# Kernel tuning notes

Measured on AMD Instinct MI355X. Metric: run time of the kernel, lower is better.

The kernel has to match this reference:

```python
import jax, jax.numpy as jnp
import numpy as np

B, N, T, D = 8, 32, 64, 64            # batch, nodes, time steps, node_dims
K, H, SO, HF = 4, 256, 256, 256       # edge_types, sep_hidden, sep_out, fusion hidden
E = N * (N - 1)                        # fully connected, no self loops


def setup_inputs() -> dict:
    key = jax.random.key(0)
    ks = jax.random.split(key, 12)
    inputs = jax.random.normal(ks[0], (B, N, T, D), jnp.float32)
    rel_type = jax.nn.softmax(jax.random.normal(ks[1], (B, E, K), jnp.float32), axis=-1)
    off = np.array([(i, j) for i in range(N) for j in range(N) if i != j])
    eye = np.eye(N, dtype=np.float32)
    send_mask = jnp.asarray(eye[off[:, 0]])  # [E, N] one-hot senders
    rec_mask = jnp.asarray(eye[off[:, 1]])   # [E, N] one-hot receivers
    s = 0.05
    W1 = jax.random.normal(ks[2], (K, 2 * D, H), jnp.float32) * s
    b1 = jnp.zeros((K, H), jnp.float32)
    W2 = jax.random.normal(ks[3], (K, H, SO), jnp.float32) * s
    b2 = jnp.zeros((K, SO), jnp.float32)
    Wf1 = jax.random.normal(ks[4], (D + SO, HF), jnp.float32) * s
    bf1 = jnp.zeros((HF,), jnp.float32)
    Wf2 = jax.random.normal(ks[5], (HF, HF), jnp.float32) * s
    bf2 = jnp.zeros((HF,), jnp.float32)
    Wf3 = jax.random.normal(ks[6], (HF, D), jnp.float32) * s
    bf3 = jnp.zeros((D,), jnp.float32)
    return dict(inputs=inputs, rel_type=rel_type, send_mask=send_mask, rec_mask=rec_mask,
                W1=W1, b1=b1, W2=W2, b2=b2, Wf1=Wf1, bf1=bf1, Wf2=Wf2, bf2=bf2,
                Wf3=Wf3, bf3=bf3, pred_steps=1)


def reference(inputs, rel_type, send_mask, rec_mask, W1, b1, W2, b2,
              Wf1, bf1, Wf2, bf2, Wf3, bf3, pred_steps):
    # inputs: [B, N, T, D] -> [B, T, N, D]
    x = jnp.swapaxes(inputs, 1, 2)
    t_full = x.shape[1]

    def one_step(node_input, rel):
        # NOTE: the original forward swaps send/rec masks when calling
        # one_step_ahead; reproduced faithfully here.
        send_b = jnp.einsum('en,btnd->bted', rec_mask, node_input)
        rec_b = jnp.einsum('en,btnd->bted', send_mask, node_input)
        edge_rep = jnp.concatenate([send_b, rec_b], axis=-1)  # [B,Tm,E,2D]
        fused = jnp.zeros(edge_rep.shape[:-1] + (SO,), edge_rep.dtype)
        for i in range(K):  # skip_first=False -> start at 0
            h = jax.nn.relu(edge_rep @ W1[i] + b1[i])
            h = jax.nn.relu(h @ W2[i] + b2[i])
            fused = fused + h * rel[..., i:i + 1]
        # aggregate edges -> nodes (original uses the swapped 'rec_mask',
        # which is forward's send_mask)
        agg = jnp.einsum('bted,en->btnd', fused, send_mask)
        aug = jnp.concatenate([node_input, agg], axis=-1)  # [B,Tm,N,D+SO]
        p = jax.nn.relu(aug @ Wf1 + bf1)
        p = jax.nn.relu(p @ Wf2 + bf2)
        p = p @ Wf3 + bf3
        return node_input + p

    last_pred = x[:, 0::pred_steps]                    # [B, Tm, N, D]
    curr_rel = jnp.broadcast_to(rel_type[:, None], (x.shape[0], t_full, E, K))[:, 0::pred_steps]
    preds = []
    for _ in range(pred_steps):
        last_pred = one_step(last_pred, curr_rel)
        preds.append(last_pred)
    # interleave preds back onto the original time grid
    stacked = jnp.stack(preds, axis=2)                 # [B, Tm, pred_steps, N, D]
    out = stacked.reshape(stacked.shape[0], -1, N, D)  # [B, Tm*pred_steps, N, D]
    pred_all = out[:, :t_full - 1]
    return jnp.swapaxes(pred_all, 1, 2)                # [B, N, T-1, D]
```

## Files before the change

### kernel.cpp

```cpp
#include <hip/hip_runtime.h>
#include <hip/hip_fp16.h>

typedef _Float16 f16;
typedef _Float16 f16x8 __attribute__((ext_vector_type(8)));
typedef _Float16 f16x4 __attribute__((ext_vector_type(4)));
typedef float    f32x4 __attribute__((ext_vector_type(4)));

#define AS1 __attribute__((address_space(1)))
#define AS3 __attribute__((address_space(3)))

__device__ __forceinline__ void gl_lds16(const void* g, void* l) {
    __builtin_amdgcn_global_load_lds((const AS1 unsigned int*)g,
                                     (AS3 unsigned int*)l, 16, 0, 0);
}

#define NB   8
#define NN   32
#define NT   64
#define ND   64
#define NK   4
#define NH   256
#define NSO  256
#define NE   992
#define TOUT 63
#define M1   (NB*TOUT*NN)
#define NBT  (NB*TOUT)

static constexpr size_t SZ_RS   = (size_t)M1 * 1024 * 2;
static constexpr size_t OFF_R   = 0;
static constexpr size_t OFF_S   = OFF_R + SZ_RS;
static constexpr size_t OFF_W2T = OFF_S + SZ_RS;
static constexpr size_t OFF_WF1 = OFF_W2T + 4*256*256*2;
static constexpr size_t OFF_WF2 = OFF_WF1 + 256*320*2;
static constexpr size_t OFF_WF3 = OFF_WF2 + 256*256*2;
static constexpr size_t OFF_REL = OFF_WF3 + 64*256*2;
static constexpr size_t OFF_AGG = OFF_REL + (size_t)NB*NN*NK*32*4;
static constexpr size_t OFF_W1T = OFF_AGG + (size_t)M1*256*4;

__global__ __launch_bounds__(256) void k0_prep(
    const float* __restrict__ W1, const float* __restrict__ W2,
    const float* __restrict__ Wf1, const float* __restrict__ Wf2,
    const float* __restrict__ Wf3, const float* __restrict__ rel,
    f16* __restrict__ W1T, f16* __restrict__ W2T, f16* __restrict__ Wf1T,
    f16* __restrict__ Wf2T, f16* __restrict__ Wf3T, float* __restrict__ REL,
    unsigned int* __restrict__ AGGZ)
{
    int id = blockIdx.x * 256 + threadIdx.x;
    if (id < 262144) {
        int k = id >> 16, co = (id >> 8) & 255, h = id & 255;
        W2T[id] = (f16)W2[k*65536 + h*256 + co];
    } else if (id < 344064) {
        int i = id - 262144; int co = i / 320, d = i % 320;
        Wf1T[i] = (f16)Wf1[d*256 + co];
    } else if (id < 409600) {
        int i = id - 344064; int co = i >> 8, h = i & 255;
        Wf2T[i] = (f16)Wf2[h*256 + co];
    } else if (id < 425984) {
        int i = id - 409600; int d = i >> 8, h = i & 255;
        Wf3T[i] = (f16)Wf3[h*64 + d];
    } else if (id < 458752) {
        int i = id - 425984;
        int j = i & 31, k = (i >> 5) & 3, ns = (i >> 7) & 31, b = i >> 12;
        float v = 0.f;
        if (j != ns) v = rel[(b*NE + ns*31 + (j < ns ? j : j - 1))*NK + k];
        REL[i] = v;
    } else {
        int i = id - 458752;
        int c = i >> 6, d = i & 63;
        int k = c >> 9, dd = (c >> 8) & 1, h = c & 255;
        W1T[i] = (f16)W1[(k*128 + dd*64 + d)*NH + h];
    }
    #pragma unroll
    for (int j = 0; j < 7; ++j) {
        int idx = id + j*589824;
        if (idx < 4128768) AGGZ[idx] = 0u;
    }
}

__global__ __launch_bounds__(256) void k1_partials(
    const float* __restrict__ inputs, const f16* __restrict__ W1T,
    const float* __restrict__ b1, f16* __restrict__ Rb, f16* __restrict__ Sb)
{
    __shared__ __align__(16) f16 xs[64][72];
    __shared__ __align__(16) f16 wl[256][72];
    int tid = threadIdx.x;
    int w = tid >> 6, lane = tid & 63, ln = lane & 15, q = lane >> 4;
    int m0 = blockIdx.x * 64;

    #pragma unroll
    for (int it = 0; it < 2; ++it) {
        int idx8 = it*256 + tid;
        int m = idx8 >> 3, hs = idx8 & 7;
        int mrow = m0 + m;
        int b = mrow / 2016, r2 = mrow % 2016, t = r2 >> 5, n = r2 & 31;
        const float* px = &inputs[((b*NN + n)*NT + t)*ND + hs*8];
        f32x4 v0 = *(const f32x4*)px, v1 = *(const f32x4*)(px + 4);
        f16x8 o;
        #pragma unroll
        for (int e = 0; e < 4; ++e) { o[e] = (f16)v0[e]; o[e+4] = (f16)v1[e]; }
        *(f16x8*)&xs[m][hs*8] = o;
    }
    const f32x4 z4 = {0.f, 0.f, 0.f, 0.f};
    for (int cc = 0; cc < 8; ++cc) {
        int k = cc >> 1, dd = cc & 1;
        __syncthreads();
        #pragma unroll
        for (int it = 0; it < 8; ++it) {
            int idx8 = it*256 + tid;
            int co = idx8 >> 3, seg = idx8 & 7;
            *(f16x8*)&wl[co][seg*8] = *(const f16x8*)&W1T[(size_t)(cc*256 + co)*64 + seg*8];
        }
        __syncthreads();
        f32x4 acc[16];
        #pragma unroll
        for (int nt = 0; nt < 16; ++nt) acc[nt] = z4;
        #pragma unroll
        for (int ks = 0; ks < 2; ++ks) {
            f16x8 Af = *(const f16x8*)&xs[w*16 + ln][ks*32 + q*8];
            #pragma unroll
            for (int nt = 0; nt < 16; ++nt) {
                f16x8 Bf = *(const f16x8*)&wl[nt*16 + ln][ks*32 + q*8];
                acc[nt] = __builtin_amdgcn_mfma_f32_16x16x32_f16(Af, Bf, acc[nt], 0, 0, 0);
            }
        }
        __syncthreads();
        f16* ob = &wl[0][0];
        #pragma unroll
        for (int nt = 0; nt < 16; ++nt) {
            int co = nt*16 + ln;
            float bias = dd ? b1[k*NH + co] : 0.f;
            #pragma unroll
            for (int r = 0; r < 4; ++r) {
                float v = acc[nt][r] + bias;
                ob[(w*16 + q*4 + r)*264 + co] = (f16)v;
            }
        }
        __syncthreads();
        f16* dst = dd ? Sb : Rb;
        #pragma unroll
        for (int it = 0; it < 8; ++it) {
            int idx8 = it*256 + tid;
            int m = idx8 >> 5, seg = idx8 & 31;
            int hcb = seg >> 3, c = seg & 7;
            *(f16x8*)&dst[(size_t)(m0 + m)*1024 + k*256 + hcb*64 + c*8] =
                *(const f16x8*)&ob[m*264 + hcb*64 + (((c ^ (m & 7))) << 3)];
        }
    }
}

__global__ __launch_bounds__(512, 2) void k2_edge(
    const f16* __restrict__ Rb, const f16* __restrict__ Sb,
    const f16* __restrict__ W2T, const float* __restrict__ b2,
    const float* __restrict__ REL, float* __restrict__ AGG)
{
    __shared__ __align__(16) f16 Rbuf[2][32*256];
    __shared__ __align__(16) f16 Sbuf[2][4*256];
    int tid = threadIdx.x;
    int blk = blockIdx.x;
    int k = blk & 3, g = blk >> 2;
    int w = tid >> 6, lane = tid & 63, ln = lane & 15, q = lane >> 4;
    int mg = w >> 2, ng = w & 3;
    int lrow = lane >> 5, lseg = lane & 31;

    f16x8 Breg[4][8];
    float bias[4];
    #pragma unroll
    for (int nt = 0; nt < 4; ++nt) {
        int co = ng*64 + nt*16 + ln;
        bias[nt] = b2[k*256 + co];
        const f16* wrow = &W2T[(size_t)(k*256 + co)*256];
        #pragma unroll
        for (int ks = 0; ks < 8; ++ks)
            Breg[nt][ks] = *(const f16x8*)&wrow[ks*32 + q*8];
    }

    auto stageR = [&](int bt, int buf) {
        #pragma unroll
        for (int it = 0; it < 2; ++it) {
            int rowbase = (w*2 + it)*2;
            gl_lds16(&Rb[((size_t)bt*NN + rowbase + lrow)*1024 + k*256 + lseg*8],
                     &Rbuf[buf][rowbase*256 + lane*8]);
        }
    };
    auto stageS = [&](int i, int buf) {
        int bt = g*8 + (i >> 3), nsq = i & 7;
        if (w < 2)
            gl_lds16(&Sb[((size_t)bt*NN + nsq*4 + w*2 + lrow)*1024 + k*256 + lseg*8],
                     &Sbuf[buf][(w*2)*256 + lane*8]);
    };

    stageR(g*8, 0);
    stageS(0, 0);
    __syncthreads();

    const f32x4 z4 = {0.f, 0.f, 0.f, 0.f};
    for (int i = 0; i < 64; ++i) {
        int ibt = i >> 3, nsq = i & 7;
        int bt = g*8 + ibt, b = bt / TOUT;
        int rb = ibt & 1, sb = i & 1;
        if (i < 63) stageS(i + 1, sb ^ 1);
        if (nsq == 6 && ibt < 7) stageR(bt + 1, rb ^ 1);

        const f16* Rl = &Rbuf[rb][0];
        const f16* Sl = &Sbuf[sb][0];
        int ns0 = nsq*4 + mg*2;
        f32x4 acc[4][4];
        #pragma unroll
        for (int mt = 0; mt < 4; ++mt)
            #pragma unroll
            for (int nt = 0; nt < 4; ++nt) acc[mt][nt] = z4;

        #pragma unroll
        for (int ks = 0; ks < 8; ++ks) {
            int hc = ks >> 1;
            int c4 = (ks & 1)*4 + q;
            int paR = hc*64 + ((c4 ^ (ln & 7)) << 3);
            f16x8 rlo = *(const f16x8*)&Rl[ln*256 + paR];
            f16x8 rhi = *(const f16x8*)&Rl[(16 + ln)*256 + paR];
            f16x8 s0 = *(const f16x8*)&Sl[(mg*2 + 0)*256 + hc*64 + ((c4 ^ (ns0 & 7)) << 3)];
            f16x8 s1 = *(const f16x8*)&Sl[(mg*2 + 1)*256 + hc*64 + ((c4 ^ ((ns0 + 1) & 7)) << 3)];
            f16x8 A[4];
            #pragma unroll
            for (int mt = 0; mt < 4; ++mt) {
                f16x8 rr = (mt & 1) ? rhi : rlo;
                f16x8 ss = (mt >> 1) ? s1 : s0;
                f16x8 v;
                #pragma unroll
                for (int e = 0; e < 8; ++e) {
                    f16 x = rr[e] + ss[e];
                    v[e] = x > (f16)0 ? x : (f16)0;
                }
                A[mt] = v;
            }
            #pragma unroll
            for (int nt = 0; nt < 4; ++nt) {
                f16x8 Bf = Breg[nt][ks];
                #pragma unroll
                for (int mt = 0; mt < 4; ++mt)
                    acc[mt][nt] = __builtin_amdgcn_mfma_f32_16x16x32_f16(
                        A[mt], Bf, acc[mt][nt], 0, 0, 0);
            }
        }
        #pragma unroll
        for (int half = 0; half < 2; ++half) {
            int ns = ns0 + half;
            const float* relp = &REL[(((size_t)b*NN + ns)*NK + k)*32];
            f32x4 rel0 = *(const f32x4*)&relp[q*4];
            f32x4 rel1 = *(const f32x4*)&relp[16 + q*4];
            #pragma unroll
            for (int nt = 0; nt < 4; ++nt) {
                float s = 0.f;
                #pragma unroll
                for (int r = 0; r < 4; ++r) {
                    float v0 = acc[2*half + 0][nt][r] + bias[nt];
                    float v1 = acc[2*half + 1][nt][r] + bias[nt];
                    v0 = v0 > 0.f ? v0 : 0.f;
                    v1 = v1 > 0.f ? v1 : 0.f;
                    s += v0 * rel0[r] + v1 * rel1[r];
                }
                s += __shfl_xor(s, 16);
                s += __shfl_xor(s, 32);
                if (lane < 16)
                    atomicAdd(&AGG[((size_t)bt*NN + ns)*256 + ng*64 + nt*16 + lane], s);
            }
        }
        __syncthreads();
    }
}

__global__ __launch_bounds__(256) void k3_node(
    const float* __restrict__ inputs, const float* __restrict__ AGG,
    const f16* __restrict__ Wf1T, const float* __restrict__ bf1,
    const f16* __restrict__ Wf2T, const float* __restrict__ bf2,
    const f16* __restrict__ Wf3T, const float* __restrict__ bf3,
    float* __restrict__ out)
{
    __shared__ __align__(16) f16 aug[64][328];
    __shared__ __align__(16) f16 p1[64][264];
    __shared__ __align__(16) f16 wl[256][72];
    int tid = threadIdx.x;
    int w = tid >> 6, lane = tid & 63, ln = lane & 15, q = lane >> 4;
    int m0 = blockIdx.x * 64;

    for (int it = 0; it < 10; ++it) {
        int s = it*256 + tid;
        if (s < 512) {
            int m = s >> 3, hs = s & 7;
            int mrow = m0 + m;
            int b = mrow / 2016, r2 = mrow % 2016, t = r2 >> 5, n = r2 & 31;
            const float* px = &inputs[((b*NN + n)*NT + t)*ND + hs*8];
            f32x4 v0 = *(const f32x4*)px, v1 = *(const f32x4*)(px + 4);
            f16x8 o;
            #pragma unroll
            for (int e = 0; e < 4; ++e) { o[e] = (f16)v0[e]; o[e+4] = (f16)v1[e]; }
            *(f16x8*)&aug[m][hs*8] = o;
        } else {
            int s2 = s - 512;
            int m = s2 >> 5, hs = s2 & 31;
            const float* pa = &AGG[(size_t)(m0 + m)*NSO + hs*8];
            f32x4 v0 = *(const f32x4*)pa, v1 = *(const f32x4*)(pa + 4);
            f16x8 o;
            #pragma unroll
            for (int e = 0; e < 4; ++e) { o[e] = (f16)v0[e]; o[e+4] = (f16)v1[e]; }
            *(f16x8*)&aug[m][64 + hs*8] = o;
        }
    }
    const f32x4 z4 = {0.f, 0.f, 0.f, 0.f};
    f32x4 acc1[16];
    #pragma unroll
    for (int nt = 0; nt < 16; ++nt) acc1[nt] = z4;
    for (int hc = 0; hc < 5; ++hc) {
        __syncthreads();
        #pragma unroll
        for (int it = 0; it < 8; ++it) {
            int idx8 = it*256 + tid;
            int co = idx8 >> 3, seg = idx8 & 7;
            *(f16x8*)&wl[co][seg*8] = *(const f16x8*)&Wf1T[co*320 + hc*64 + seg*8];
        }
        __syncthreads();
        #pragma unroll
        for (int ks = 0; ks < 2; ++ks) {
            f16x8 Af = *(const f16x8*)&aug[w*16 + ln][hc*64 + ks*32 + q*8];
            #pragma unroll
            for (int nt = 0; nt < 16; ++nt) {
                f16x8 Bf = *(const f16x8*)&wl[nt*16 + ln][ks*32 + q*8];
                acc1[nt] = __builtin_amdgcn_mfma_f32_16x16x32_f16(Af, Bf, acc1[nt], 0, 0, 0);
            }
        }
    }
    #pragma unroll
    for (int nt = 0; nt < 16; ++nt) {
        int co = nt*16 + ln;
        float bias = bf1[co];
        #pragma unroll
        for (int r = 0; r < 4; ++r) {
            float v = acc1[nt][r] + bias; v = v > 0.f ? v : 0.f;
            p1[w*16 + q*4 + r][co] = (f16)v;
        }
    }
    f32x4 acc2[16];
    #pragma unroll
    for (int nt = 0; nt < 16; ++nt) acc2[nt] = z4;
    for (int hc = 0; hc < 4; ++hc) {
        __syncthreads();
        #pragma unroll
        for (int it = 0; it < 8; ++it) {
            int idx8 = it*256 + tid;
            int co = idx8 >> 3, seg = idx8 & 7;
            *(f16x8*)&wl[co][seg*8] = *(const f16x8*)&Wf2T[co*256 + hc*64 + seg*8];
        }
        __syncthreads();
        #pragma unroll
        for (int ks = 0; ks < 2; ++ks) {
            f16x8 Af = *(const f16x8*)&p1[w*16 + ln][hc*64 + ks*32 + q*8];
            #pragma unroll
            for (int nt = 0; nt < 16; ++nt) {
                f16x8 Bf = *(const f16x8*)&wl[nt*16 + ln][ks*32 + q*8];
                acc2[nt] = __builtin_amdgcn_mfma_f32_16x16x32_f16(Af, Bf, acc2[nt], 0, 0, 0);
            }
        }
    }
    f16* p2 = &aug[0][0];
    #pragma unroll
    for (int nt = 0; nt < 16; ++nt) {
        int co = nt*16 + ln;
        float bias = bf2[co];
        #pragma unroll
        for (int r = 0; r < 4; ++r) {
            float v = acc2[nt][r] + bias; v = v > 0.f ? v : 0.f;
            p2[(w*16 + q*4 + r)*264 + co] = (f16)v;
        }
    }
    __syncthreads();
    f16* w3 = &wl[0][0];
    #pragma unroll
    for (int it = 0; it < 8; ++it) {
        int idx8 = it*256 + tid;
        int d = idx8 >> 5, seg = idx8 & 31;
        *(f16x8*)&w3[d*264 + seg*8] = *(const f16x8*)&Wf3T[d*256 + seg*8];
    }
    __syncthreads();
    f32x4 acc3[4];
    #pragma unroll
    for (int nt = 0; nt < 4; ++nt) acc3[nt] = z4;
    #pragma unroll
    for (int ks = 0; ks < 8; ++ks) {
        f16x8 Af = *(const f16x8*)&p2[(w*16 + ln)*264 + ks*32 + q*8];
        #pragma unroll
        for (int nt = 0; nt < 4; ++nt) {
            f16x8 Bf = *(const f16x8*)&w3[(nt*16 + ln)*264 + ks*32 + q*8];
            acc3[nt] = __builtin_amdgcn_mfma_f32_16x16x32_f16(Af, Bf, acc3[nt], 0, 0, 0);
        }
    }
    #pragma unroll
    for (int nt = 0; nt < 4; ++nt) {
        int d = nt*16 + ln;
        float bias = bf3[d];
        #pragma unroll
        for (int r = 0; r < 4; ++r) {
            int mrow = m0 + w*16 + q*4 + r;
            int b = mrow / 2016, r2 = mrow % 2016, t = r2 >> 5, n = r2 & 31;
            float xv = inputs[((b*NN + n)*NT + t)*ND + d];
            out[((size_t)(b*NN + n)*TOUT + t)*ND + d] = acc3[nt][r] + bias + xv;
        }
    }
}

extern "C" void kernel_launch(void* const* d_in, const int* in_sizes, int n_in,
                              void* d_out, int out_size, void* d_ws, size_t ws_size,
                              hipStream_t stream)
{
    const float* inputs = (const float*)d_in[0];
    const float* rel    = (const float*)d_in[1];
    const float* W1     = (const float*)d_in[4];
    const float* b1     = (const float*)d_in[5];
    const float* W2     = (const float*)d_in[6];
    const float* b2     = (const float*)d_in[7];
    const float* Wf1    = (const float*)d_in[8];
    const float* bf1    = (const float*)d_in[9];
    const float* Wf2    = (const float*)d_in[10];
    const float* bf2    = (const float*)d_in[11];
    const float* Wf3    = (const float*)d_in[12];
    const float* bf3    = (const float*)d_in[13];
    char* ws = (char*)d_ws;
    f16*   Rb   = (f16*)(ws + OFF_R);
    f16*   Sb   = (f16*)(ws + OFF_S);
    f16*   W2T  = (f16*)(ws + OFF_W2T);
    f16*   Wf1T = (f16*)(ws + OFF_WF1);
    f16*   Wf2T = (f16*)(ws + OFF_WF2);
    f16*   Wf3T = (f16*)(ws + OFF_WF3);
    float* REL  = (float*)(ws + OFF_REL);
    float* AGG  = (float*)(ws + OFF_AGG);
    f16*   W1T  = (f16*)(ws + OFF_W1T);
    float* out  = (float*)d_out;

    hipLaunchKernelGGL(k0_prep, dim3(2304), dim3(256), 0, stream,
                       W1, W2, Wf1, Wf2, Wf3, rel, W1T, W2T, Wf1T, Wf2T, Wf3T, REL,
                       (unsigned int*)AGG);
    hipLaunchKernelGGL(k1_partials, dim3(252), dim3(256), 0, stream,
                       inputs, W1T, b1, Rb, Sb);
    hipLaunchKernelGGL(k2_edge, dim3(252), dim3(512), 0, stream,
                       Rb, Sb, W2T, b2, REL, AGG);
    hipLaunchKernelGGL(k3_node, dim3(252), dim3(256), 0, stream,
                       inputs, AGG, Wf1T, bf1, Wf2T, bf2, Wf3T, bf3, out);
}
```

Baseline: 458.2 us.

## Split edge kernel into 256-thread blocks over half the time steps; vectorize ReLU

The edge-MLP kernel now runs 504 blocks of 4 waves instead of 252 blocks of 8 waves. Each block covers 4 time steps instead of 8 and processes two sender nodes per iteration across 16 iterations per time step. The ReLU on (R+S) is rewritten as a vector elementwise max, aiming for packed f16 ops. The goal is better load balance across the CUs and lower per-block register and LDS pressure. The cost is that each block reloads the W2 weights into registers over twice as many blocks, and R tiles are staged twice as often relative to the compute done.

```diff
diff --git a/kernel.cpp b/kernel.cpp
--- a/kernel.cpp
+++ b/kernel.cpp
@@ -148,18 +148,17 @@
     }
 }
 
-__global__ __launch_bounds__(512, 2) void k2_edge(
+__global__ __launch_bounds__(256, 2) void k2_edge(
     const f16* __restrict__ Rb, const f16* __restrict__ Sb,
     const f16* __restrict__ W2T, const float* __restrict__ b2,
     const float* __restrict__ REL, float* __restrict__ AGG)
 {
     __shared__ __align__(16) f16 Rbuf[2][32*256];
-    __shared__ __align__(16) f16 Sbuf[2][4*256];
+    __shared__ __align__(16) f16 Sbuf[2][2*256];
     int tid = threadIdx.x;
     int blk = blockIdx.x;
     int k = blk & 3, g = blk >> 2;
-    int w = tid >> 6, lane = tid & 63, ln = lane & 15, q = lane >> 4;
-    int mg = w >> 2, ng = w & 3;
+    int ng = tid >> 6, lane = tid & 63, ln = lane & 15, q = lane >> 4;
     int lrow = lane >> 5, lseg = lane & 31;
 
     f16x8 Breg[4][8];
@@ -176,34 +175,35 @@
 
     auto stageR = [&](int bt, int buf) {
         #pragma unroll
-        for (int it = 0; it < 2; ++it) {
-            int rowbase = (w*2 + it)*2;
+        for (int it = 0; it < 4; ++it) {
+            int rowbase = ng*8 + it*2;
             gl_lds16(&Rb[((size_t)bt*NN + rowbase + lrow)*1024 + k*256 + lseg*8],
                      &Rbuf[buf][rowbase*256 + lane*8]);
         }
     };
     auto stageS = [&](int i, int buf) {
-        int bt = g*8 + (i >> 3), nsq = i & 7;
-        if (w < 2)
-            gl_lds16(&Sb[((size_t)bt*NN + nsq*4 + w*2 + lrow)*1024 + k*256 + lseg*8],
-                     &Sbuf[buf][(w*2)*256 + lane*8]);
+        int bt = g*4 + (i >> 4), nsp = i & 15;
+        if (ng == 0)
+            gl_lds16(&Sb[((size_t)bt*NN + nsp*2 + lrow)*1024 + k*256 + lseg*8],
+                     &Sbuf[buf][lane*8]);
     };
 
-    stageR(g*8, 0);
+    stageR(g*4, 0);
     stageS(0, 0);
     __syncthreads();
 
     const f32x4 z4 = {0.f, 0.f, 0.f, 0.f};
+    const f16x8 zf = {0,0,0,0,0,0,0,0};
     for (int i = 0; i < 64; ++i) {
-        int ibt = i >> 3, nsq = i & 7;
-        int bt = g*8 + ibt, b = bt / TOUT;
+        int ibt = i >> 4, nsp = i & 15;
+        int bt = g*4 + ibt, b = bt / TOUT;
         int rb = ibt & 1, sb = i & 1;
         if (i < 63) stageS(i + 1, sb ^ 1);
-        if (nsq == 6 && ibt < 7) stageR(bt + 1, rb ^ 1);
+        if (nsp == 14 && ibt < 3) stageR(bt + 1, rb ^ 1);
 
         const f16* Rl = &Rbuf[rb][0];
         const f16* Sl = &Sbuf[sb][0];
-        int ns0 = nsq*4 + mg*2;
+        int ns0 = nsp*2;
         f32x4 acc[4][4];
         #pragma unroll
         for (int mt = 0; mt < 4; ++mt)
@@ -217,21 +217,13 @@
             int paR = hc*64 + ((c4 ^ (ln & 7)) << 3);
             f16x8 rlo = *(const f16x8*)&Rl[ln*256 + paR];
             f16x8 rhi = *(const f16x8*)&Rl[(16 + ln)*256 + paR];
-            f16x8 s0 = *(const f16x8*)&Sl[(mg*2 + 0)*256 + hc*64 + ((c4 ^ (ns0 & 7)) << 3)];
-            f16x8 s1 = *(const f16x8*)&Sl[(mg*2 + 1)*256 + hc*64 + ((c4 ^ ((ns0 + 1) & 7)) << 3)];
+            f16x8 s0 = *(const f16x8*)&Sl[0*256 + hc*64 + ((c4 ^ (ns0 & 7)) << 3)];
+            f16x8 s1 = *(const f16x8*)&Sl[1*256 + hc*64 + ((c4 ^ ((ns0 + 1) & 7)) << 3)];
             f16x8 A[4];
-            #pragma unroll
-            for (int mt = 0; mt < 4; ++mt) {
-                f16x8 rr = (mt & 1) ? rhi : rlo;
-                f16x8 ss = (mt >> 1) ? s1 : s0;
-                f16x8 v;
-                #pragma unroll
-                for (int e = 0; e < 8; ++e) {
-                    f16 x = rr[e] + ss[e];
-                    v[e] = x > (f16)0 ? x : (f16)0;
-                }
-                A[mt] = v;
-            }
+            A[0] = __builtin_elementwise_max(rlo + s0, zf);
+            A[1] = __builtin_elementwise_max(rhi + s0, zf);
+            A[2] = __builtin_elementwise_max(rlo + s1, zf);
+            A[3] = __builtin_elementwise_max(rhi + s1, zf);
             #pragma unroll
             for (int nt = 0; nt < 4; ++nt) {
                 f16x8 Bf = Breg[nt][ks];
@@ -439,7 +431,7 @@
                        (unsigned int*)AGG);
     hipLaunchKernelGGL(k1_partials, dim3(252), dim3(256), 0, stream,
                        inputs, W1T, b1, Rb, Sb);
-    hipLaunchKernelGGL(k2_edge, dim3(252), dim3(512), 0, stream,
+    hipLaunchKernelGGL(k2_edge, dim3(504), dim3(256), 0, stream,
                        Rb, Sb, W2T, b2, REL, AGG);
     hipLaunchKernelGGL(k3_node, dim3(252), dim3(256), 0, stream,
                        inputs, AGG, Wf1T, bf1, Wf2T, bf2, Wf3T, bf3, out);
```

After: 464.2 us. Within noise of the previous version (+1.3%).

## Double-buffer weight tiles via direct global-to-LDS loads with pre-swizzled layouts

Applied to the files above, without the earlier changes.

Weight matrices for k1 and k3 are stored pre-swizzled in the prep kernel, so they can be streamed into double-buffered LDS with global_load_lds while the MFMA loop works on the other buffer. This removes register-staged copies, LDS padding and one barrier per chunk. In k2 the bias moves into the accumulator's initial value and the add-relu runs as packed vector fp16 max. The cost is extra LDS for the second buffer, which may lower occupancy. The XOR swizzle on both the write and read sides must stay consistent.

```diff
diff --git a/kernel.cpp b/kernel.cpp
--- a/kernel.cpp
+++ b/kernel.cpp
@@ -41,8 +41,8 @@
     const float* __restrict__ W1, const float* __restrict__ W2,
     const float* __restrict__ Wf1, const float* __restrict__ Wf2,
     const float* __restrict__ Wf3, const float* __restrict__ rel,
-    f16* __restrict__ W1T, f16* __restrict__ W2T, f16* __restrict__ Wf1T,
-    f16* __restrict__ Wf2T, f16* __restrict__ Wf3T, float* __restrict__ REL,
+    f16* __restrict__ W1TS, f16* __restrict__ W2T, f16* __restrict__ Wf1TS,
+    f16* __restrict__ Wf2TS, f16* __restrict__ Wf3TS, float* __restrict__ REL,
     unsigned int* __restrict__ AGGZ)
 {
     int id = blockIdx.x * 256 + threadIdx.x;
@@ -50,14 +50,20 @@
         int k = id >> 16, co = (id >> 8) & 255, h = id & 255;
         W2T[id] = (f16)W2[k*65536 + h*256 + co];
     } else if (id < 344064) {
-        int i = id - 262144; int co = i / 320, d = i % 320;
-        Wf1T[i] = (f16)Wf1[d*256 + co];
+        int i = id - 262144; int co = i / 320, dcol = i % 320;
+        int hc = dcol >> 6, c8 = (dcol >> 3) & 7, e = dcol & 7;
+        int sd = hc*64 + ((c8 ^ (co & 7)) << 3) + e;
+        Wf1TS[i] = (f16)Wf1[sd*256 + co];
     } else if (id < 409600) {
-        int i = id - 344064; int co = i >> 8, h = i & 255;
-        Wf2T[i] = (f16)Wf2[h*256 + co];
+        int i = id - 344064; int co = i >> 8, dcol = i & 255;
+        int hc = dcol >> 6, c8 = (dcol >> 3) & 7, e = dcol & 7;
+        int sh = hc*64 + ((c8 ^ (co & 7)) << 3) + e;
+        Wf2TS[i] = (f16)Wf2[sh*256 + co];
     } else if (id < 425984) {
-        int i = id - 409600; int d = i >> 8, h = i & 255;
-        Wf3T[i] = (f16)Wf3[h*64 + d];
+        int i = id - 409600; int d = i >> 8, col = i & 255;
+        int c32 = col >> 3, e = col & 7;
+        int sc = (c32 & 24) | ((c32 & 7) ^ (d & 7));
+        Wf3TS[i] = (f16)Wf3[(sc*8 + e)*64 + d];
     } else if (id < 458752) {
         int i = id - 425984;
         int j = i & 31, k = (i >> 5) & 3, ns = (i >> 7) & 31, b = i >> 12;
@@ -66,9 +72,11 @@
         REL[i] = v;
     } else {
         int i = id - 458752;
-        int c = i >> 6, d = i & 63;
+        int c = i >> 6, dcol = i & 63;
+        int c8 = (dcol >> 3) & 7, e = dcol & 7;
+        int sd = ((c8 ^ (c & 7)) << 3) + e;
         int k = c >> 9, dd = (c >> 8) & 1, h = c & 255;
-        W1T[i] = (f16)W1[(k*128 + dd*64 + d)*NH + h];
+        W1TS[i] = (f16)W1[(k*128 + dd*64 + sd)*NH + h];
     }
     #pragma unroll
     for (int j = 0; j < 7; ++j) {
@@ -78,13 +86,15 @@
 }
 
 __global__ __launch_bounds__(256) void k1_partials(
-    const float* __restrict__ inputs, const f16* __restrict__ W1T,
+    const float* __restrict__ inputs, const f16* __restrict__ W1TS,
     const float* __restrict__ b1, f16* __restrict__ Rb, f16* __restrict__ Sb)
 {
     __shared__ __align__(16) f16 xs[64][72];
-    __shared__ __align__(16) f16 wl[256][72];
+    __shared__ __align__(16) f16 wl[2][256*64];
+    __shared__ __align__(16) f16 ob[64*264];
     int tid = threadIdx.x;
     int w = tid >> 6, lane = tid & 63, ln = lane & 15, q = lane >> 4;
+    int lrow8 = lane >> 3, lc8 = lane & 7;
     int m0 = blockIdx.x * 64;
 
     #pragma unroll
@@ -100,17 +110,22 @@
         for (int e = 0; e < 4; ++e) { o[e] = (f16)v0[e]; o[e+4] = (f16)v1[e]; }
         *(f16x8*)&xs[m][hs*8] = o;
     }
+    auto stageW = [&](int cc, int buf) {
+        #pragma unroll
+        for (int it = 0; it < 8; ++it) {
+            int co0 = (it*4 + w)*8;
+            gl_lds16(&W1TS[(size_t)(cc*256 + co0 + lrow8)*64 + lc8*8],
+                     &wl[buf][co0*64 + lane*8]);
+        }
+    };
+    stageW(0, 0);
+    __syncthreads();
+
     const f32x4 z4 = {0.f, 0.f, 0.f, 0.f};
     for (int cc = 0; cc < 8; ++cc) {
         int k = cc >> 1, dd = cc & 1;
-        __syncthreads();
-        #pragma unroll
-        for (int it = 0; it < 8; ++it) {
-            int idx8 = it*256 + tid;
-            int co = idx8 >> 3, seg = idx8 & 7;
-            *(f16x8*)&wl[co][seg*8] = *(const f16x8*)&W1T[(size_t)(cc*256 + co)*64 + seg*8];
-        }
-        __syncthreads();
+        if (cc < 7) stageW(cc + 1, (cc + 1) & 1);
+        const f16* wb = &wl[cc & 1][0];
         f32x4 acc[16];
         #pragma unroll
         for (int nt = 0; nt < 16; ++nt) acc[nt] = z4;
@@ -119,12 +134,11 @@
             f16x8 Af = *(const f16x8*)&xs[w*16 + ln][ks*32 + q*8];
             #pragma unroll
             for (int nt = 0; nt < 16; ++nt) {
-                f16x8 Bf = *(const f16x8*)&wl[nt*16 + ln][ks*32 + q*8];
+                f16x8 Bf = *(const f16x8*)&wb[(nt*16 + ln)*64 +
+                                (((ks*4 + q) ^ (ln & 7)) << 3)];
                 acc[nt] = __builtin_amdgcn_mfma_f32_16x16x32_f16(Af, Bf, acc[nt], 0, 0, 0);
             }
         }
-        __syncthreads();
-        f16* ob = &wl[0][0];
         #pragma unroll
         for (int nt = 0; nt < 16; ++nt) {
             int co = nt*16 + ln;
@@ -145,6 +159,7 @@
             *(f16x8*)&dst[(size_t)(m0 + m)*1024 + k*256 + hcb*64 + c*8] =
                 *(const f16x8*)&ob[m*264 + hcb*64 + (((c ^ (m & 7))) << 3)];
         }
+        __syncthreads();
     }
 }
 
@@ -163,11 +178,13 @@
     int lrow = lane >> 5, lseg = lane & 31;
 
     f16x8 Breg[4][8];
-    float bias[4];
+    f32x4 bini[4];
     #pragma unroll
     for (int nt = 0; nt < 4; ++nt) {
         int co = ng*64 + nt*16 + ln;
-        bias[nt] = b2[k*256 + co];
+        float bv = b2[k*256 + co];
+        f32x4 bb = {bv, bv, bv, bv};
+        bini[nt] = bb;
         const f16* wrow = &W2T[(size_t)(k*256 + co)*256];
         #pragma unroll
         for (int ks = 0; ks < 8; ++ks)
@@ -193,7 +210,7 @@
     stageS(0, 0);
     __syncthreads();
 
-    const f32x4 z4 = {0.f, 0.f, 0.f, 0.f};
+    const f16x8 zf = {0,0,0,0,0,0,0,0};
     for (int i = 0; i < 64; ++i) {
         int ibt = i >> 3, nsq = i & 7;
         int bt = g*8 + ibt, b = bt / TOUT;
@@ -208,7 +225,7 @@
         #pragma unroll
         for (int mt = 0; mt < 4; ++mt)
             #pragma unroll
-            for (int nt = 0; nt < 4; ++nt) acc[mt][nt] = z4;
+            for (int nt = 0; nt < 4; ++nt) acc[mt][nt] = bini[nt];
 
         #pragma unroll
         for (int ks = 0; ks < 8; ++ks) {
@@ -220,18 +237,10 @@
             f16x8 s0 = *(const f16x8*)&Sl[(mg*2 + 0)*256 + hc*64 + ((c4 ^ (ns0 & 7)) << 3)];
             f16x8 s1 = *(const f16x8*)&Sl[(mg*2 + 1)*256 + hc*64 + ((c4 ^ ((ns0 + 1) & 7)) << 3)];
             f16x8 A[4];
-            #pragma unroll
-            for (int mt = 0; mt < 4; ++mt) {
-                f16x8 rr = (mt & 1) ? rhi : rlo;
-                f16x8 ss = (mt >> 1) ? s1 : s0;
-                f16x8 v;
-                #pragma unroll
-                for (int e = 0; e < 8; ++e) {
-                    f16 x = rr[e] + ss[e];
-                    v[e] = x > (f16)0 ? x : (f16)0;
-                }
-                A[mt] = v;
-            }
+            A[0] = __builtin_elementwise_max(rlo + s0, zf);
+            A[1] = __builtin_elementwise_max(rhi + s0, zf);
+            A[2] = __builtin_elementwise_max(rlo + s1, zf);
+            A[3] = __builtin_elementwise_max(rhi + s1, zf);
             #pragma unroll
             for (int nt = 0; nt < 4; ++nt) {
                 f16x8 Bf = Breg[nt][ks];
@@ -252,8 +261,8 @@
                 float s = 0.f;
                 #pragma unroll
                 for (int r = 0; r < 4; ++r) {
-                    float v0 = acc[2*half + 0][nt][r] + bias[nt];
-                    float v1 = acc[2*half + 1][nt][r] + bias[nt];
+                    float v0 = acc[2*half + 0][nt][r];
+                    float v1 = acc[2*half + 1][nt][r];
                     v0 = v0 > 0.f ? v0 : 0.f;
                     v1 = v1 > 0.f ? v1 : 0.f;
                     s += v0 * rel0[r] + v1 * rel1[r];
@@ -270,16 +279,17 @@
 
 __global__ __launch_bounds__(256) void k3_node(
     const float* __restrict__ inputs, const float* __restrict__ AGG,
-    const f16* __restrict__ Wf1T, const float* __restrict__ bf1,
-    const f16* __restrict__ Wf2T, const float* __restrict__ bf2,
-    const f16* __restrict__ Wf3T, const float* __restrict__ bf3,
+    const f16* __restrict__ Wf1TS, const float* __restrict__ bf1,
+    const f16* __restrict__ Wf2TS, const float* __restrict__ bf2,
+    const f16* __restrict__ Wf3TS, const float* __restrict__ bf3,
     float* __restrict__ out)
 {
     __shared__ __align__(16) f16 aug[64][328];
     __shared__ __align__(16) f16 p1[64][264];
-    __shared__ __align__(16) f16 wl[256][72];
+    __shared__ __align__(16) f16 wl[2][256*64];
     int tid = threadIdx.x;
     int w = tid >> 6, lane = tid & 63, ln = lane & 15, q = lane >> 4;
+    int lrow8 = lane >> 3, lc8 = lane & 7;
     int m0 = blockIdx.x * 64;
 
     for (int it = 0; it < 10; ++it) {
@@ -305,28 +315,45 @@
             *(f16x8*)&aug[m][64 + hs*8] = o;
         }
     }
+    auto stageW1 = [&](int hc, int buf) {
+        #pragma unroll
+        for (int it = 0; it < 8; ++it) {
+            int co0 = (it*4 + w)*8;
+            gl_lds16(&Wf1TS[(size_t)(co0 + lrow8)*320 + hc*64 + lc8*8],
+                     &wl[buf][co0*64 + lane*8]);
+        }
+    };
+    auto stageW2 = [&](int hc, int buf) {
+        #pragma unroll
+        for (int it = 0; it < 8; ++it) {
+            int co0 = (it*4 + w)*8;
+            gl_lds16(&Wf2TS[(size_t)(co0 + lrow8)*256 + hc*64 + lc8*8],
+                     &wl[buf][co0*64 + lane*8]);
+        }
+    };
+    stageW1(0, 0);
+    __syncthreads();
+
     const f32x4 z4 = {0.f, 0.f, 0.f, 0.f};
     f32x4 acc1[16];
     #pragma unroll
     for (int nt = 0; nt < 16; ++nt) acc1[nt] = z4;
     for (int hc = 0; hc < 5; ++hc) {
-        __syncthreads();
-        #pragma unroll
-        for (int it = 0; it < 8; ++it) {
-            int idx8 = it*256 + tid;
-            int co = idx8 >> 3, seg = idx8 & 7;
-            *(f16x8*)&wl[co][seg*8] = *(const f16x8*)&Wf1T[co*320 + hc*64 + seg*8];
-        }
-        __syncthreads();
+        int buf = hc & 1;
+        if (hc < 4) stageW1(hc + 1, buf ^ 1);
+        else        stageW2(0, buf ^ 1);
+        const f16* wb = &wl[buf][0];
         #pragma unroll
         for (int ks = 0; ks < 2; ++ks) {
             f16x8 Af = *(const f16x8*)&aug[w*16 + ln][hc*64 + ks*32 + q*8];
             #pragma unroll
             for (int nt = 0; nt < 16; ++nt) {
-                f16x8 Bf = *(const f16x8*)&wl[nt*16 + ln][ks*32 + q*8];
+                f16x8 Bf = *(const f16x8*)&wb[(nt*16 + ln)*64 +
+                                (((ks*4 + q) ^ (ln & 7)) << 3)];
                 acc1[nt] = __builtin_amdgcn_mfma_f32_16x16x32_f16(Af, Bf, acc1[nt], 0, 0, 0);
             }
         }
+        __syncthreads();
     }
     #pragma unroll
     for (int nt = 0; nt < 16; ++nt) {
@@ -342,23 +369,20 @@
     #pragma unroll
     for (int nt = 0; nt < 16; ++nt) acc2[nt] = z4;
     for (int hc = 0; hc < 4; ++hc) {
-        __syncthreads();
-        #pragma unroll
-        for (int it = 0; it < 8; ++it) {
-            int idx8 = it*256 + tid;
-            int co = idx8 >> 3, seg = idx8 & 7;
-            *(f16x8*)&wl[co][seg*8] = *(const f16x8*)&Wf2T[co*256 + hc*64 + seg*8];
-        }
-        __syncthreads();
+        int buf = (hc + 1) & 1;
+        if (hc < 3) stageW2(hc + 1, buf ^ 1);
+        const f16* wb = &wl[buf][0];
         #pragma unroll
         for (int ks = 0; ks < 2; ++ks) {
             f16x8 Af = *(const f16x8*)&p1[w*16 + ln][hc*64 + ks*32 + q*8];
             #pragma unroll
             for (int nt = 0; nt < 16; ++nt) {
-                f16x8 Bf = *(const f16x8*)&wl[nt*16 + ln][ks*32 + q*8];
+                f16x8 Bf = *(const f16x8*)&wb[(nt*16 + ln)*64 +
+                                (((ks*4 + q) ^ (ln & 7)) << 3)];
                 acc2[nt] = __builtin_amdgcn_mfma_f32_16x16x32_f16(Af, Bf, acc2[nt], 0, 0, 0);
             }
         }
+        __syncthreads();
     }
     f16* p2 = &aug[0][0];
     #pragma unroll
@@ -371,13 +395,14 @@
             p2[(w*16 + q*4 + r)*264 + co] = (f16)v;
         }
     }
-    __syncthreads();
-    f16* w3 = &wl[0][0];
-    #pragma unroll
-    for (int it = 0; it < 8; ++it) {
-        int idx8 = it*256 + tid;
-        int d = idx8 >> 5, seg = idx8 & 31;
-        *(f16x8*)&w3[d*264 + seg*8] = *(const f16x8*)&Wf3T[d*256 + seg*8];
+    {
+        #pragma unroll
+        for (int it = 0; it < 8; ++it) {
+            int d0 = (it*4 + w)*2;
+            int lr = lane >> 5, ls = lane & 31;
+            gl_lds16(&Wf3TS[(size_t)(d0 + lr)*256 + ls*8],
+                     &wl[0][d0*256 + lane*8]);
+        }
     }
     __syncthreads();
     f32x4 acc3[4];
@@ -388,7 +413,9 @@
         f16x8 Af = *(const f16x8*)&p2[(w*16 + ln)*264 + ks*32 + q*8];
         #pragma unroll
         for (int nt = 0; nt < 4; ++nt) {
-            f16x8 Bf = *(const f16x8*)&w3[(nt*16 + ln)*264 + ks*32 + q*8];
+            int pos = ks*4 + q;
+            int phys = (pos & 24) | ((pos & 7) ^ (ln & 7));
+            f16x8 Bf = *(const f16x8*)&wl[0][(nt*16 + ln)*256 + phys*8];
             acc3[nt] = __builtin_amdgcn_mfma_f32_16x16x32_f16(Af, Bf, acc3[nt], 0, 0, 0);
         }
     }
@@ -423,24 +450,24 @@
     const float* Wf3    = (const float*)d_in[12];
     const float* bf3    = (const float*)d_in[13];
     char* ws = (char*)d_ws;
-    f16*   Rb   = (f16*)(ws + OFF_R);
-    f16*   Sb   = (f16*)(ws + OFF_S);
-    f16*   W2T  = (f16*)(ws + OFF_W2T);
-    f16*   Wf1T = (f16*)(ws + OFF_WF1);
-    f16*   Wf2T = (f16*)(ws + OFF_WF2);
-    f16*   Wf3T = (f16*)(ws + OFF_WF3);
-    float* REL  = (float*)(ws + OFF_REL);
-    float* AGG  = (float*)(ws + OFF_AGG);
-    f16*   W1T  = (f16*)(ws + OFF_W1T);
-    float* out  = (float*)d_out;
+    f16*   Rb    = (f16*)(ws + OFF_R);
+    f16*   Sb    = (f16*)(ws + OFF_S);
+    f16*   W2T   = (f16*)(ws + OFF_W2T);
+    f16*   Wf1TS = (f16*)(ws + OFF_WF1);
+    f16*   Wf2TS = (f16*)(ws + OFF_WF2);
+    f16*   Wf3TS = (f16*)(ws + OFF_WF3);
+    float* REL   = (float*)(ws + OFF_REL);
+    float* AGG   = (float*)(ws + OFF_AGG);
+    f16*   W1TS  = (f16*)(ws + OFF_W1T);
+    float* out   = (float*)d_out;
 
     hipLaunchKernelGGL(k0_prep, dim3(2304), dim3(256), 0, stream,
-                       W1, W2, Wf1, Wf2, Wf3, rel, W1T, W2T, Wf1T, Wf2T, Wf3T, REL,
+                       W1, W2, Wf1, Wf2, Wf3, rel, W1TS, W2T, Wf1TS, Wf2TS, Wf3TS, REL,
                        (unsigned int*)AGG);
     hipLaunchKernelGGL(k1_partials, dim3(252), dim3(256), 0, stream,
-                       inputs, W1T, b1, Rb, Sb);
+                       inputs, W1TS, b1, Rb, Sb);
     hipLaunchKernelGGL(k2_edge, dim3(252), dim3(512), 0, stream,
                        Rb, Sb, W2T, b2, REL, AGG);
     hipLaunchKernelGGL(k3_node, dim3(252), dim3(256), 0, stream,
-                       inputs, AGG, Wf1T, bf1, Wf2T, bf2, Wf3T, bf3, out);
-}
+                       inputs, AGG, Wf1TS, bf1, Wf2TS, bf2, Wf3TS, bf3, out);
+}
```

Result: no change. 450.4 us (-1.7%).
